# Kernel optimization log

Hardware: AMD Instinct MI355X
Metric: run time of the kernel (lower is better)

The kernel has to match this reference:

```python
import jax, jax.numpy as jnp
import numpy as np

B, SQ, SK = 2, 2048, 2048
D = 1024            # in_features == num_heads * head_size
H, HS = 16, 64      # num_heads, head_size
SCALE = HS ** -0.5


def setup_inputs() -> dict:
    key = jax.random.key(0)
    ks = jax.random.split(key, 10)
    s = 0.02
    return {
        "inputs": jax.random.normal(ks[0], (B, SQ, D), jnp.float32),
        "context": jax.random.normal(ks[1], (B, SK, D), jnp.float32),
        "Wq": jax.random.normal(ks[2], (D, D), jnp.float32) * s,
        "bq": jnp.zeros((D,), jnp.float32),
        "Wk": jax.random.normal(ks[3], (D, D), jnp.float32) * s,
        "bk": jnp.zeros((D,), jnp.float32),
        "Wv": jax.random.normal(ks[4], (D, D), jnp.float32) * s,
        "bv": jnp.zeros((D,), jnp.float32),
        "Wo": jax.random.normal(ks[5], (D, D), jnp.float32) * s,
        "bo": jnp.zeros((D,), jnp.float32),
    }


def reference(inputs, context, Wq, bq, Wk, bk, Wv, bv, Wo, bo):
    # QKV projections (torch Linear: x @ W.T + b; here W stored as [in, out])
    q = inputs @ Wq + bq            # [B, SQ, D]
    k = context @ Wk + bk           # [B, SK, D]
    v = context @ Wv + bv           # [B, SK, D]
    q = q.reshape(B, SQ, H, HS)
    k = k.reshape(B, SK, H, HS)
    v = v.reshape(B, SK, H, HS)
    # scores: [B, H, SQ, SK] -- full score matrix materialized (as in source)
    score = jnp.einsum("bqhd,bkhd->bhqk", q, k) * SCALE
    weights = jax.nn.softmax(score, axis=-1)
    attn = jnp.einsum("bhqk,bkhd->bqhd", weights, v)  # [B, SQ, H, HS]
    out = attn.reshape(B, SQ, H * HS)
    return out @ Wo + bo
```

## Files before the change

### kernel.cpp

```cpp
#include <hip/hip_runtime.h>

#define BB 2
#define SQ 2048
#define SK 2048
#define DD 1024
#define HH 16
#define HS 64
#define SCALE 0.125f
#define LOG2E 1.4426950408889634f

typedef __bf16 bf16x8 __attribute__((ext_vector_type(8)));
typedef float f32x4 __attribute__((ext_vector_type(4)));
typedef unsigned int uint;

#if defined(__has_builtin)
#if __has_builtin(__builtin_amdgcn_exp2f)
#define FEXP2(x) __builtin_amdgcn_exp2f(x)
#endif
#endif
#ifndef FEXP2
extern "C" __device__ float __ocml_native_exp2_f32(float);
#define FEXP2(x) __ocml_native_exp2_f32(x)
#endif

__device__ __forceinline__ void gload_lds16(const __bf16* g, __bf16* l) {
    __builtin_amdgcn_global_load_lds((const __attribute__((address_space(1))) uint*)(g),
                                     (__attribute__((address_space(3))) uint*)(l), 16, 0, 0);
}

__global__ void wtrans(const float* __restrict__ W0, const float* __restrict__ W1,
                       const float* __restrict__ W2, const float* __restrict__ W3,
                       __bf16* __restrict__ Wt) {
    __shared__ __bf16 tile[32][33];
    const float* W = blockIdx.z == 0 ? W0 : blockIdx.z == 1 ? W1 : blockIdx.z == 2 ? W2 : W3;
    __bf16* out = Wt + (size_t)blockIdx.z * DD * DD;
    int tx = threadIdx.x, ty = threadIdx.y;
    int k0 = blockIdx.y * 32, n0 = blockIdx.x * 32;
#pragma unroll
    for (int j = 0; j < 4; ++j)
        tile[ty + j * 8][tx] = (__bf16)W[(size_t)(k0 + ty + j * 8) * DD + n0 + tx];
    __syncthreads();
#pragma unroll
    for (int j = 0; j < 4; ++j)
        out[(size_t)(n0 + ty + j * 8) * DD + k0 + tx] = tile[tx][ty + j * 8];
}

#define BM 128
#define BN2 64
#define BK 64
template <int MODE>
__device__ __forceinline__ void gemm_body(__bf16 (* __restrict__ As)[BK], __bf16 (* __restrict__ Bs)[BK],
                                          const float* __restrict__ Af, const __bf16* __restrict__ Bt,
                                          const float* __restrict__ bias, void* __restrict__ Cout,
                                          float scale) {
    int t = threadIdx.x;
    int w = t >> 6, l = t & 63;
    int lm = l & 15, lk = l >> 4;
    int wr = w >> 1, wc = w & 1;
    int flat = blockIdx.x + 16 * blockIdx.y;
    int nf = (flat & 7) * 64 + (flat >> 3);
    int bc = nf & 15, br = nf >> 4;
    int srow = l >> 3, sc8 = l & 7;

    const float* ag = Af + (size_t)(br * BM + w * 32 + srow) * 1024 + sc8 * 8;
    __bf16* aw = &As[w * 32 + srow][(sc8 ^ srow) * 8];

    float4 xa0, xa1, xb0, xb1, xc0, xc1, xd0, xd1;
#define GA_LOAD(KT)                                                                   \
    xa0 = *(const float4*)(ag + (KT));          xa1 = *(const float4*)(ag + (KT) + 4);\
    xb0 = *(const float4*)(ag + 8192 + (KT));   xb1 = *(const float4*)(ag + 8192 + (KT) + 4);\
    xc0 = *(const float4*)(ag + 16384 + (KT));  xc1 = *(const float4*)(ag + 16384 + (KT) + 4);\
    xd0 = *(const float4*)(ag + 24576 + (KT));  xd1 = *(const float4*)(ag + 24576 + (KT) + 4);
#define GA_WRITE()                                                                    \
    {                                                                                 \
        bf16x8 va = {(__bf16)xa0.x, (__bf16)xa0.y, (__bf16)xa0.z, (__bf16)xa0.w,      \
                     (__bf16)xa1.x, (__bf16)xa1.y, (__bf16)xa1.z, (__bf16)xa1.w};     \
        bf16x8 vb = {(__bf16)xb0.x, (__bf16)xb0.y, (__bf16)xb0.z, (__bf16)xb0.w,      \
                     (__bf16)xb1.x, (__bf16)xb1.y, (__bf16)xb1.z, (__bf16)xb1.w};     \
        bf16x8 vc = {(__bf16)xc0.x, (__bf16)xc0.y, (__bf16)xc0.z, (__bf16)xc0.w,      \
                     (__bf16)xc1.x, (__bf16)xc1.y, (__bf16)xc1.z, (__bf16)xc1.w};     \
        bf16x8 vd = {(__bf16)xd0.x, (__bf16)xd0.y, (__bf16)xd0.z, (__bf16)xd0.w,      \
                     (__bf16)xd1.x, (__bf16)xd1.y, (__bf16)xd1.z, (__bf16)xd1.w};     \
        *(bf16x8*)(aw)        = va;                                                   \
        *(bf16x8*)(aw + 512)  = vb;                                                   \
        *(bf16x8*)(aw + 1024) = vc;                                                   \
        *(bf16x8*)(aw + 1536) = vd;                                                   \
    }

    f32x4 acc[4][2] = {};
    GA_LOAD(0);
    for (int kt = 0; kt < 1024; kt += BK) {
        __syncthreads();
        GA_WRITE();
#pragma unroll
        for (int j = 0; j < 2; ++j) {
            int r0 = (w * 2 + j) * 8;
            gload_lds16(&Bt[(size_t)(bc * BN2 + r0 + srow) * 1024 + kt + sc8 * 8], &Bs[r0][0]);
        }
        __syncthreads();
        if (kt + BK < 1024) { GA_LOAD(kt + BK); }
#pragma unroll
        for (int kk = 0; kk < BK; kk += 32) {
            bf16x8 af[4], bf[2];
#pragma unroll
            for (int m = 0; m < 4; ++m)
                af[m] = *(const bf16x8*)&As[wr * 64 + m * 16 + lm][((((kk >> 3) + lk)) ^ (lm & 7)) * 8];
#pragma unroll
            for (int n = 0; n < 2; ++n) bf[n] = *(const bf16x8*)&Bs[wc * 32 + n * 16 + lm][kk + lk * 8];
#pragma unroll
            for (int m = 0; m < 4; ++m)
#pragma unroll
                for (int n = 0; n < 2; ++n)
                    acc[m][n] = __builtin_amdgcn_mfma_f32_16x16x32_bf16(af[m], bf[n], acc[m][n], 0, 0, 0);
        }
    }
#pragma unroll
    for (int m = 0; m < 4; ++m)
#pragma unroll
        for (int n = 0; n < 2; ++n) {
            int col = bc * BN2 + wc * 32 + n * 16 + lm;
            float bv = bias[col];
            if constexpr (MODE == 2) {
                int row = br * BM + wr * 64 + m * 16 + lk * 4;
                int b_ = row >> 11, sk = row & 2047;
                int skb = sk & ~63, o = sk & 63;
                int p0 = (o & 32) | (((o >> 3) & 1) << 4) | (((o >> 2) & 1) << 3) | (((o >> 4) & 1) << 2);
                int h_ = col >> 6, d_ = col & 63;
                union { ushort4 u; __bf16 h[4]; } pk;
#pragma unroll
                for (int r = 0; r < 4; ++r) pk.h[r] = (__bf16)(acc[m][n][r] + bv);
                *(ushort4*)((__bf16*)Cout + ((size_t)((b_ * 16 + h_) * 64 + d_) * 2048 + skb + p0)) = pk.u;
            } else {
#pragma unroll
                for (int r = 0; r < 4; ++r) {
                    int row = br * BM + wr * 64 + m * 16 + lk * 4 + r;
                    ((__bf16*)Cout)[(size_t)row * 1024 + col] = (__bf16)((acc[m][n][r] + bv) * scale);
                }
            }
        }
#undef GA_LOAD
#undef GA_WRITE
}

__global__ __launch_bounds__(256) void gemm_qkv(const float* __restrict__ Ain, const float* __restrict__ Actx,
                                                const __bf16* __restrict__ Wt,
                                                const float* __restrict__ bq, const float* __restrict__ bk,
                                                const float* __restrict__ bv,
                                                __bf16* __restrict__ Qb, __bf16* __restrict__ Kb,
                                                __bf16* __restrict__ Vtb, float qscale) {
    __shared__ __bf16 As[BM][BK];
    __shared__ __bf16 Bs[BN2][BK];
    int z = blockIdx.z;
    const float* A = (z == 0) ? Ain : Actx;
    const __bf16* B = Wt + (size_t)z * DD * DD;
    if (z == 0)      gemm_body<0>(As, Bs, A, B, bq, Qb, qscale);
    else if (z == 1) gemm_body<0>(As, Bs, A, B, bk, Kb, 1.f);
    else             gemm_body<2>(As, Bs, A, B, bv, Vtb, 1.f);
}

__global__ __launch_bounds__(256) void gemm_out64(const __bf16* __restrict__ A, const __bf16* __restrict__ Bt,
                                                  const float* __restrict__ bias, float* __restrict__ C) {
    __shared__ __bf16 As[64][64];
    __shared__ __bf16 Bs[128][64];
    int t = threadIdx.x;
    int w = t >> 6, l = t & 63;
    int lm = l & 15, lk = l >> 4;
    int flat = blockIdx.x + 8 * blockIdx.y;
    int nf = (flat & 7) * 64 + (flat >> 3);
    int bc = nf & 7, br = nf >> 3;
    int srow = (l >> 3), scol = (l & 7) * 8;
    f32x4 acc[4][2] = {};
    for (int kt = 0; kt < 1024; kt += 64) {
        __syncthreads();
#pragma unroll
        for (int j = 0; j < 2; ++j) {
            int r0 = (j * 4 + w) * 8;
            gload_lds16(&A[(size_t)(br * 64 + r0 + srow) * 1024 + kt + scol], &As[r0][0]);
        }
#pragma unroll
        for (int j = 0; j < 4; ++j) {
            int r0 = (j * 4 + w) * 8;
            gload_lds16(&Bt[(size_t)(bc * 128 + r0 + srow) * 1024 + kt + scol], &Bs[r0][0]);
        }
        __syncthreads();
#pragma unroll
        for (int kk = 0; kk < 64; kk += 32) {
            bf16x8 af[4], bf[2];
#pragma unroll
            for (int m = 0; m < 4; ++m) af[m] = *(const bf16x8*)&As[m * 16 + lm][kk + lk * 8];
#pragma unroll
            for (int n = 0; n < 2; ++n) bf[n] = *(const bf16x8*)&Bs[w * 32 + n * 16 + lm][kk + lk * 8];
#pragma unroll
            for (int m = 0; m < 4; ++m)
#pragma unroll
                for (int n = 0; n < 2; ++n)
                    acc[m][n] = __builtin_amdgcn_mfma_f32_16x16x32_bf16(af[m], bf[n], acc[m][n], 0, 0, 0);
        }
    }
#pragma unroll
    for (int m = 0; m < 4; ++m)
#pragma unroll
        for (int n = 0; n < 2; ++n) {
            int col = bc * 128 + w * 32 + n * 16 + lm;
            float bv = bias[col];
#pragma unroll
            for (int r = 0; r < 4; ++r) {
                int row = br * 64 + m * 16 + lk * 4 + r;
                C[(size_t)row * 1024 + col] = acc[m][n][r] + bv;
            }
        }
}

__global__ __launch_bounds__(512) void flash_attn(const __bf16* __restrict__ Q,
                                                  const __bf16* __restrict__ Kb,
                                                  const __bf16* __restrict__ Vt,
                                                  __bf16* __restrict__ O) {
    __shared__ __bf16 Ks[2][64 * 64];
    __shared__ __bf16 Vs[2][64 * 64];
    int t = threadIdx.x, w = t >> 6, l = t & 63;
    int lm = l & 15, lk = l >> 4;
    int flat = blockIdx.x + 16 * blockIdx.y;
    int nf = (flat & 7) * 64 + (flat >> 3);
    int bh = nf >> 4, b = bh >> 4, h = bh & 15;
    int q0 = (nf & 15) * 128;

    bf16x8 qf[2];
#pragma unroll
    for (int kk = 0; kk < 2; ++kk)
        qf[kk] = *(const bf16x8*)&Q[(size_t)(b * SQ + q0 + w * 16 + lm) * DD + h * HS + kk * 32 + lk * 8];

    int r0 = t >> 3, c8 = t & 7;
    int chs = c8 ^ (r0 & 7);
    __bf16* ksl0 = &Ks[0][r0 * 64 + chs * 8];
    __bf16* vsl0 = &Vs[0][r0 * 64 + chs * 8];

    const __bf16* kp0 = Kb + (size_t)b * SK * DD + h * HS + (size_t)r0 * DD + c8 * 8;
    const __bf16* vp0 = Vt + (size_t)bh * HS * SK + (size_t)r0 * SK + c8 * 8;

    int o0 = lm * 64 + ((lk ^ (lm & 7)) * 8);
    int o1 = lm * 64 + (((4 + lk) ^ (lm & 7)) * 8);

    float4 kr0, vr0;
#define FA_LOAD()                                                                \
    kr0 = *(const float4*)kp0; vr0 = *(const float4*)vp0;                        \
    kp0 += (size_t)64 * DD; vp0 += 64;
#define FA_WRITE(BUF)                                                            \
    *(float4*)(ksl0 + (BUF) * 4096) = kr0;                                       \
    *(float4*)(vsl0 + (BUF) * 4096) = vr0;

    FA_LOAD();
    FA_WRITE(0);
    __syncthreads();

    bf16x8 ones;
#pragma unroll
    for (int j = 0; j < 8; ++j) ones[j] = (__bf16)1.0f;

    f32x4 o[4] = {};
    f32x4 o_s = {};

    for (int it = 0; it < 32; ++it) {
        int buf = it & 1;
        if (it + 1 < 32) { FA_LOAD(); }

        const __bf16* KsB = &Ks[buf][0];
        const __bf16* VsB = &Vs[buf][0];

        f32x4 st[4] = {};
        __builtin_amdgcn_s_setprio(1);
#pragma unroll
        for (int kk = 0; kk < 2; ++kk) {
#pragma unroll
            for (int n = 0; n < 4; ++n) {
                bf16x8 kf = *(const bf16x8*)&KsB[(kk ? o1 : o0) + n * 1024];
                st[n] = __builtin_amdgcn_mfma_f32_16x16x32_bf16(kf, qf[kk], st[n], 0, 0, 0);
            }
        }
        __builtin_amdgcn_s_setprio(0);

#pragma unroll
        for (int kk = 0; kk < 2; ++kk) {
            bf16x8 pa;
#pragma unroll
            for (int j = 0; j < 8; ++j)
                pa[j] = (__bf16)FEXP2(st[2 * kk + (j >> 2)][j & 3]);
            __builtin_amdgcn_s_setprio(1);
            o_s = __builtin_amdgcn_mfma_f32_16x16x32_bf16(pa, ones, o_s, 0, 0, 0);
#pragma unroll
            for (int dn = 0; dn < 4; ++dn) {
                bf16x8 vf = *(const bf16x8*)&VsB[(kk ? o1 : o0) + dn * 1024];
                o[dn] = __builtin_amdgcn_mfma_f32_16x16x32_bf16(pa, vf, o[dn], 0, 0, 0);
            }
            __builtin_amdgcn_s_setprio(0);
        }

        if (it + 1 < 32) { FA_WRITE(buf ^ 1); }
        __syncthreads();
    }

    f32x4 inv;
#pragma unroll
    for (int r = 0; r < 4; ++r) inv[r] = 1.f / o_s[r];
#pragma unroll
    for (int dn = 0; dn < 4; ++dn)
#pragma unroll
        for (int r = 0; r < 4; ++r) {
            int row = q0 + w * 16 + lk * 4 + r;
            int col = h * HS + dn * 16 + lm;
            O[(size_t)(b * SQ + row) * DD + col] = (__bf16)(o[dn][r] * inv[r]);
        }
}

extern "C" void kernel_launch(void* const* d_in, const int* in_sizes, int n_in,
                              void* d_out, int out_size, void* d_ws, size_t ws_size,
                              hipStream_t stream) {
    const float* inputs  = (const float*)d_in[0];
    const float* context = (const float*)d_in[1];
    const float* Wq = (const float*)d_in[2];
    const float* bq = (const float*)d_in[3];
    const float* Wk = (const float*)d_in[4];
    const float* bk = (const float*)d_in[5];
    const float* Wv = (const float*)d_in[6];
    const float* bv = (const float*)d_in[7];
    const float* Wo = (const float*)d_in[8];
    const float* bo = (const float*)d_in[9];
    float* out = (float*)d_out;

    char* ws = (char*)d_ws;
    const size_t SEG = (size_t)4096 * 1024 * sizeof(__bf16);
    __bf16* attb = (__bf16*)(ws + 0 * SEG);
    __bf16* Wt   = (__bf16*)(ws + 2 * SEG);
    __bf16* Qb   = (__bf16*)(ws + 3 * SEG);
    __bf16* Kbuf = (__bf16*)(ws + 4 * SEG);
    __bf16* Vtb  = (__bf16*)(ws + 5 * SEG);

    wtrans<<<dim3(32, 32, 4), dim3(32, 8), 0, stream>>>(Wq, Wk, Wv, Wo, Wt);

    gemm_qkv<<<dim3(16, 32, 3), 256, 0, stream>>>(inputs, context, Wt, bq, bk, bv,
                                                  Qb, Kbuf, Vtb, SCALE * LOG2E);

    flash_attn<<<dim3(16, 32), 512, 0, stream>>>(Qb, Kbuf, Vtb, attb);

    gemm_out64<<<dim3(8, 64), 256, 0, stream>>>(attb, Wt + (size_t)3 * DD * DD, bo, out);
}
```

Measured before the change: 124.8 us.

## Fuse K and V projections per tile, retile QKV GEMM, pre-swizzle weights

The QKV GEMM is restructured so that each K/V block computes both the K and V projections from a single loaded context tile, which halves how often the fp32 context activations are read and converted. The tile becomes 64x128 instead of 128x64, and Q blocks take 128 output columns. The weight transpose now writes an XOR-swizzled layout so B tiles can be staged with plain vector copies through registers while avoiding LDS bank conflicts. The output GEMM reads its B tile with the matching swizzle. The risk is lower overlap from the register-staged B loads and extra branching between Q and K/V blocks.

```diff
diff --git a/kernel.cpp b/kernel.cpp
--- a/kernel.cpp
+++ b/kernel.cpp
@@ -41,121 +41,149 @@
         tile[ty + j * 8][tx] = (__bf16)W[(size_t)(k0 + ty + j * 8) * DD + n0 + tx];
     __syncthreads();
 #pragma unroll
-    for (int j = 0; j < 4; ++j)
-        out[(size_t)(n0 + ty + j * 8) * DD + k0 + tx] = tile[tx][ty + j * 8];
-}
-
-#define BM 128
-#define BN2 64
-#define BK 64
-template <int MODE>
-__device__ __forceinline__ void gemm_body(__bf16 (* __restrict__ As)[BK], __bf16 (* __restrict__ Bs)[BK],
-                                          const float* __restrict__ Af, const __bf16* __restrict__ Bt,
-                                          const float* __restrict__ bias, void* __restrict__ Cout,
-                                          float scale) {
-    int t = threadIdx.x;
-    int w = t >> 6, l = t & 63;
+    for (int j = 0; j < 4; ++j) {
+        int n = n0 + ty + j * 8;
+        int k = k0 + tx;
+        int kswz = (k & ~63) | ((((k >> 3) ^ n) & 7) << 3) | (k & 7);
+        out[(size_t)n * DD + kswz] = tile[tx][ty + j * 8];
+    }
+}
+
+__global__ __launch_bounds__(256, 4) void gemm_qkv(
+        const float* __restrict__ Ain, const float* __restrict__ Actx,
+        const __bf16* __restrict__ Wt,
+        const float* __restrict__ bq, const float* __restrict__ bk, const float* __restrict__ bv,
+        __bf16* __restrict__ Qb, __bf16* __restrict__ Kb, __bf16* __restrict__ Vtb,
+        float qscale) {
+    __shared__ __bf16 As[64][64];
+    __shared__ __bf16 Bs[128][64];
+    int t = threadIdx.x, w = t >> 6, l = t & 63;
     int lm = l & 15, lk = l >> 4;
     int wr = w >> 1, wc = w & 1;
     int flat = blockIdx.x + 16 * blockIdx.y;
-    int nf = (flat & 7) * 64 + (flat >> 3);
-    int bc = nf & 15, br = nf >> 4;
-    int srow = l >> 3, sc8 = l & 7;
-
-    const float* ag = Af + (size_t)(br * BM + w * 32 + srow) * 1024 + sc8 * 8;
-    __bf16* aw = &As[w * 32 + srow][(sc8 ^ srow) * 8];
-
-    float4 xa0, xa1, xb0, xb1, xc0, xc1, xd0, xd1;
-#define GA_LOAD(KT)                                                                   \
-    xa0 = *(const float4*)(ag + (KT));          xa1 = *(const float4*)(ag + (KT) + 4);\
-    xb0 = *(const float4*)(ag + 8192 + (KT));   xb1 = *(const float4*)(ag + 8192 + (KT) + 4);\
-    xc0 = *(const float4*)(ag + 16384 + (KT));  xc1 = *(const float4*)(ag + 16384 + (KT) + 4);\
-    xd0 = *(const float4*)(ag + 24576 + (KT));  xd1 = *(const float4*)(ag + 24576 + (KT) + 4);
-#define GA_WRITE()                                                                    \
+    int nf = (flat & 7) * 192 + (flat >> 3);
+    bool isQ = nf < 512;
+    int bc, br;
+    if (isQ) { bc = nf & 7; br = nf >> 3; }
+    else     { int f = nf - 512; bc = f & 15; br = f >> 4; }
+
+    int ra = t >> 2, ca = (t & 3) * 2;
+    const float* ag = (isQ ? Ain : Actx) + (size_t)(br * 64 + ra) * 1024 + ca * 8;
+    __bf16* aw0 = &As[ra][((ca)     ^ (ra & 7)) * 8];
+    __bf16* aw1 = &As[ra][((ca + 1) ^ (ra & 7)) * 8];
+
+    int rb = t >> 3, c8 = t & 7;
+    const __bf16 *bg0, *bg1, *bg2, *bg3;
+    if (isQ) {
+        const __bf16* Wq_ = Wt;
+        bg0 = Wq_ + (size_t)(bc * 128 + rb)      * 1024 + c8 * 8;
+        bg1 = Wq_ + (size_t)(bc * 128 + rb + 32) * 1024 + c8 * 8;
+        bg2 = Wq_ + (size_t)(bc * 128 + rb + 64) * 1024 + c8 * 8;
+        bg3 = Wq_ + (size_t)(bc * 128 + rb + 96) * 1024 + c8 * 8;
+    } else {
+        const __bf16* Wk_ = Wt + (size_t)DD * DD;
+        const __bf16* Wv_ = Wt + (size_t)2 * DD * DD;
+        bg0 = Wk_ + (size_t)(bc * 64 + rb)      * 1024 + c8 * 8;
+        bg1 = Wk_ + (size_t)(bc * 64 + rb + 32) * 1024 + c8 * 8;
+        bg2 = Wv_ + (size_t)(bc * 64 + rb)      * 1024 + c8 * 8;
+        bg3 = Wv_ + (size_t)(bc * 64 + rb + 32) * 1024 + c8 * 8;
+    }
+    __bf16* bw0 = &Bs[rb][c8 * 8];
+    __bf16* bw1 = &Bs[rb + 32][c8 * 8];
+    __bf16* bw2 = &Bs[rb + 64][c8 * 8];
+    __bf16* bw3 = &Bs[rb + 96][c8 * 8];
+
+    int brow[4];
+#pragma unroll
+    for (int n = 0; n < 4; ++n)
+        brow[n] = isQ ? (wc * 64 + n * 16 + lm)
+                      : ((n >> 1) * 64 + wc * 32 + (n & 1) * 16 + lm);
+
+    float4 xa0, xa1, xa2, xa3, xb0, xb1, xb2, xb3;
+#define G_LOAD()                                                                      \
+    xa0 = *(const float4*)(ag);     xa1 = *(const float4*)(ag + 4);                   \
+    xa2 = *(const float4*)(ag + 8); xa3 = *(const float4*)(ag + 12);                  \
+    xb0 = *(const float4*)bg0; xb1 = *(const float4*)bg1;                             \
+    xb2 = *(const float4*)bg2; xb3 = *(const float4*)bg3;                             \
+    ag += 64; bg0 += 64; bg1 += 64; bg2 += 64; bg3 += 64;
+#define G_WRITE()                                                                     \
     {                                                                                 \
-        bf16x8 va = {(__bf16)xa0.x, (__bf16)xa0.y, (__bf16)xa0.z, (__bf16)xa0.w,      \
-                     (__bf16)xa1.x, (__bf16)xa1.y, (__bf16)xa1.z, (__bf16)xa1.w};     \
-        bf16x8 vb = {(__bf16)xb0.x, (__bf16)xb0.y, (__bf16)xb0.z, (__bf16)xb0.w,      \
-                     (__bf16)xb1.x, (__bf16)xb1.y, (__bf16)xb1.z, (__bf16)xb1.w};     \
-        bf16x8 vc = {(__bf16)xc0.x, (__bf16)xc0.y, (__bf16)xc0.z, (__bf16)xc0.w,      \
-                     (__bf16)xc1.x, (__bf16)xc1.y, (__bf16)xc1.z, (__bf16)xc1.w};     \
-        bf16x8 vd = {(__bf16)xd0.x, (__bf16)xd0.y, (__bf16)xd0.z, (__bf16)xd0.w,      \
-                     (__bf16)xd1.x, (__bf16)xd1.y, (__bf16)xd1.z, (__bf16)xd1.w};     \
-        *(bf16x8*)(aw)        = va;                                                   \
-        *(bf16x8*)(aw + 512)  = vb;                                                   \
-        *(bf16x8*)(aw + 1024) = vc;                                                   \
-        *(bf16x8*)(aw + 1536) = vd;                                                   \
-    }
-
-    f32x4 acc[4][2] = {};
-    GA_LOAD(0);
-    for (int kt = 0; kt < 1024; kt += BK) {
-        __syncthreads();
-        GA_WRITE();
-#pragma unroll
-        for (int j = 0; j < 2; ++j) {
-            int r0 = (w * 2 + j) * 8;
-            gload_lds16(&Bt[(size_t)(bc * BN2 + r0 + srow) * 1024 + kt + sc8 * 8], &Bs[r0][0]);
-        }
-        __syncthreads();
-        if (kt + BK < 1024) { GA_LOAD(kt + BK); }
-#pragma unroll
-        for (int kk = 0; kk < BK; kk += 32) {
-            bf16x8 af[4], bf[2];
-#pragma unroll
-            for (int m = 0; m < 4; ++m)
-                af[m] = *(const bf16x8*)&As[wr * 64 + m * 16 + lm][((((kk >> 3) + lk)) ^ (lm & 7)) * 8];
-#pragma unroll
-            for (int n = 0; n < 2; ++n) bf[n] = *(const bf16x8*)&Bs[wc * 32 + n * 16 + lm][kk + lk * 8];
-#pragma unroll
-            for (int m = 0; m < 4; ++m)
-#pragma unroll
-                for (int n = 0; n < 2; ++n)
+        bf16x8 va0 = {(__bf16)xa0.x, (__bf16)xa0.y, (__bf16)xa0.z, (__bf16)xa0.w,     \
+                      (__bf16)xa1.x, (__bf16)xa1.y, (__bf16)xa1.z, (__bf16)xa1.w};    \
+        bf16x8 va1 = {(__bf16)xa2.x, (__bf16)xa2.y, (__bf16)xa2.z, (__bf16)xa2.w,     \
+                      (__bf16)xa3.x, (__bf16)xa3.y, (__bf16)xa3.z, (__bf16)xa3.w};    \
+        *(bf16x8*)aw0 = va0; *(bf16x8*)aw1 = va1;                                     \
+        *(float4*)bw0 = xb0; *(float4*)bw1 = xb1;                                     \
+        *(float4*)bw2 = xb2; *(float4*)bw3 = xb3;                                     \
+    }
+
+    f32x4 acc[2][4] = {};
+    G_LOAD();
+    for (int kt = 0; kt < 1024; kt += 64) {
+        __syncthreads();
+        G_WRITE();
+        __syncthreads();
+        if (kt + 64 < 1024) { G_LOAD(); }
+#pragma unroll
+        for (int kk = 0; kk < 64; kk += 32) {
+            int ch = ((kk >> 3) + lk);
+            bf16x8 af[2], bf[4];
+#pragma unroll
+            for (int m = 0; m < 2; ++m)
+                af[m] = *(const bf16x8*)&As[wr * 32 + m * 16 + lm][(ch ^ (lm & 7)) * 8];
+#pragma unroll
+            for (int n = 0; n < 4; ++n)
+                bf[n] = *(const bf16x8*)&Bs[brow[n]][(ch ^ (lm & 7)) * 8];
+#pragma unroll
+            for (int m = 0; m < 2; ++m)
+#pragma unroll
+                for (int n = 0; n < 4; ++n)
                     acc[m][n] = __builtin_amdgcn_mfma_f32_16x16x32_bf16(af[m], bf[n], acc[m][n], 0, 0, 0);
         }
     }
-#pragma unroll
-    for (int m = 0; m < 4; ++m)
-#pragma unroll
-        for (int n = 0; n < 2; ++n) {
-            int col = bc * BN2 + wc * 32 + n * 16 + lm;
-            float bv = bias[col];
-            if constexpr (MODE == 2) {
-                int row = br * BM + wr * 64 + m * 16 + lk * 4;
-                int b_ = row >> 11, sk = row & 2047;
-                int skb = sk & ~63, o = sk & 63;
-                int p0 = (o & 32) | (((o >> 3) & 1) << 4) | (((o >> 2) & 1) << 3) | (((o >> 4) & 1) << 2);
-                int h_ = col >> 6, d_ = col & 63;
-                union { ushort4 u; __bf16 h[4]; } pk;
-#pragma unroll
-                for (int r = 0; r < 4; ++r) pk.h[r] = (__bf16)(acc[m][n][r] + bv);
-                *(ushort4*)((__bf16*)Cout + ((size_t)((b_ * 16 + h_) * 64 + d_) * 2048 + skb + p0)) = pk.u;
-            } else {
+#undef G_LOAD
+#undef G_WRITE
+
+    if (isQ) {
+#pragma unroll
+        for (int m = 0; m < 2; ++m)
+#pragma unroll
+            for (int n = 0; n < 4; ++n) {
+                int col = bc * 128 + wc * 64 + n * 16 + lm;
+                float bb = bq[col];
 #pragma unroll
                 for (int r = 0; r < 4; ++r) {
-                    int row = br * BM + wr * 64 + m * 16 + lk * 4 + r;
-                    ((__bf16*)Cout)[(size_t)row * 1024 + col] = (__bf16)((acc[m][n][r] + bv) * scale);
+                    int row = br * 64 + wr * 32 + m * 16 + lk * 4 + r;
+                    Qb[(size_t)row * 1024 + col] = (__bf16)((acc[m][n][r] + bb) * qscale);
                 }
             }
-        }
-#undef GA_LOAD
-#undef GA_WRITE
-}
-
-__global__ __launch_bounds__(256) void gemm_qkv(const float* __restrict__ Ain, const float* __restrict__ Actx,
-                                                const __bf16* __restrict__ Wt,
-                                                const float* __restrict__ bq, const float* __restrict__ bk,
-                                                const float* __restrict__ bv,
-                                                __bf16* __restrict__ Qb, __bf16* __restrict__ Kb,
-                                                __bf16* __restrict__ Vtb, float qscale) {
-    __shared__ __bf16 As[BM][BK];
-    __shared__ __bf16 Bs[BN2][BK];
-    int z = blockIdx.z;
-    const float* A = (z == 0) ? Ain : Actx;
-    const __bf16* B = Wt + (size_t)z * DD * DD;
-    if (z == 0)      gemm_body<0>(As, Bs, A, B, bq, Qb, qscale);
-    else if (z == 1) gemm_body<0>(As, Bs, A, B, bk, Kb, 1.f);
-    else             gemm_body<2>(As, Bs, A, B, bv, Vtb, 1.f);
+    } else {
+#pragma unroll
+        for (int m = 0; m < 2; ++m)
+#pragma unroll
+            for (int n = 0; n < 4; ++n) {
+                int col = bc * 64 + wc * 32 + (n & 1) * 16 + lm;
+                if (n < 2) {
+                    float bb = bk[col];
+#pragma unroll
+                    for (int r = 0; r < 4; ++r) {
+                        int row = br * 64 + wr * 32 + m * 16 + lk * 4 + r;
+                        Kb[(size_t)row * 1024 + col] = (__bf16)(acc[m][n][r] + bb);
+                    }
+                } else {
+                    float bb = bv[col];
+                    int row = br * 64 + wr * 32 + m * 16 + lk * 4;
+                    int b_ = row >> 11, sk = row & 2047;
+                    int skb = sk & ~63, o = sk & 63;
+                    int p0 = (o & 32) | (((o >> 3) & 1) << 4) | (((o >> 2) & 1) << 3) | (((o >> 4) & 1) << 2);
+                    int h_ = col >> 6, d_ = col & 63;
+                    union { ushort4 u; __bf16 hh[4]; } pk;
+#pragma unroll
+                    for (int r = 0; r < 4; ++r) pk.hh[r] = (__bf16)(acc[m][n][r] + bb);
+                    *(ushort4*)(Vtb + ((size_t)((b_ * 16 + h_) * 64 + d_) * 2048 + skb + p0)) = pk.u;
+                }
+            }
+    }
 }
 
 __global__ __launch_bounds__(256) void gemm_out64(const __bf16* __restrict__ A, const __bf16* __restrict__ Bt,
@@ -185,11 +213,13 @@
         __syncthreads();
 #pragma unroll
         for (int kk = 0; kk < 64; kk += 32) {
+            int ch = ((kk >> 3) + lk);
             bf16x8 af[4], bf[2];
 #pragma unroll
             for (int m = 0; m < 4; ++m) af[m] = *(const bf16x8*)&As[m * 16 + lm][kk + lk * 8];
 #pragma unroll
-            for (int n = 0; n < 2; ++n) bf[n] = *(const bf16x8*)&Bs[w * 32 + n * 16 + lm][kk + lk * 8];
+            for (int n = 0; n < 2; ++n)
+                bf[n] = *(const bf16x8*)&Bs[w * 32 + n * 16 + lm][(ch ^ (lm & 7)) * 8];
 #pragma unroll
             for (int m = 0; m < 4; ++m)
 #pragma unroll
@@ -336,8 +366,8 @@
 
     wtrans<<<dim3(32, 32, 4), dim3(32, 8), 0, stream>>>(Wq, Wk, Wv, Wo, Wt);
 
-    gemm_qkv<<<dim3(16, 32, 3), 256, 0, stream>>>(inputs, context, Wt, bq, bk, bv,
-                                                  Qb, Kbuf, Vtb, SCALE * LOG2E);
+    gemm_qkv<<<dim3(16, 96), 256, 0, stream>>>(inputs, context, Wt, bq, bk, bv,
+                                               Qb, Kbuf, Vtb, SCALE * LOG2E);
 
     flash_attn<<<dim3(16, 32), 512, 0, stream>>>(Qb, Kbuf, Vtb, attb);
 
```

After: 113.8 us. 8.8% less time.
